# Kernel optimization log

Measured on AMD Instinct MI355X. Metric: run time of the kernel, lower is better.

## Reference

```python
import jax, jax.numpy as jnp
import numpy as np

B, N, D_IN, D_OUT, MAX_POS = 256, 256, 768, 300, 256
NEG_INF = -9e15
LEAKY_SLOPE = 0.2


def setup_inputs() -> dict:
    key = jax.random.key(0)
    ks = jax.random.split(key, 6)
    h = jax.random.normal(ks[0], (B, N, D_IN), dtype=jnp.float32)
    adj = (jax.random.uniform(ks[1], (B, N, N)) > 0.9).astype(jnp.float32)
    adj = jnp.maximum(adj, jnp.eye(N, dtype=jnp.float32)[None])
    positions = jax.random.randint(ks[2], (B, N), 0, MAX_POS)
    W = jax.random.normal(ks[3], (D_IN, D_OUT), dtype=jnp.float32) * (1.0 / np.sqrt(D_IN))
    a_src = jax.random.normal(ks[4], (1, D_OUT), dtype=jnp.float32) * 0.05
    a_dst = jax.random.normal(ks[5], (1, D_OUT), dtype=jnp.float32) * 0.05
    pos_table = jax.random.normal(jax.random.fold_in(key, 7), (MAX_POS, D_OUT), dtype=jnp.float32)
    return {"h": h, "adj": adj, "positions": positions, "W": W,
            "a_src": a_src, "a_dst": a_dst, "pos_table": pos_table}


def reference(h, adj, positions, W, a_src, a_dst, pos_table):
    # Wh = W(h) + position embedding          [B, N, D_OUT]
    Wh = jnp.einsum('bni,io->bno', h, W) + pos_table[positions]
    # additive attention scores
    f_src = jnp.einsum('bno,o->bn', Wh, a_src[0])  # [B, N]
    f_dst = jnp.einsum('bno,o->bn', Wh, a_dst[0])  # [B, N]
    e = f_src[:, :, None] + f_dst[:, None, :]      # [B, N, N]
    e = jnp.where(e >= 0, e, LEAKY_SLOPE * e)      # LeakyReLU(0.2)
    # adjacency masking + softmax over last dim
    masked = jnp.where(adj > 0, e, NEG_INF)
    attention = jax.nn.softmax(masked, axis=-1)
    # (eval mode: edge dropout and dropout are identity)
    h_prime = jnp.einsum('bnm,bmo->bno', attention, Wh)
    return h_prime, attention
```

## Files before the change

kernel.cpp:

```cpp
#include <hip/hip_runtime.h>

#define B_    256
#define N_    256
#define DIN   768
#define DOUT  300
#define DOUTP 320
#define M_    (B_*N_)
#define HP_ELEMS (M_*DOUT)
#define NEG_INF -9.0e15f

typedef _Float16 f16;
typedef __attribute__((ext_vector_type(8))) _Float16 f16x8;
typedef __attribute__((ext_vector_type(4))) _Float16 f16x4;
typedef __attribute__((ext_vector_type(4))) float    f32x4;

__device__ __forceinline__ void async_copy16(void* lds, const void* g) {
    __builtin_amdgcn_global_load_lds(
        (const __attribute__((address_space(1))) void*)g,
        (__attribute__((address_space(3))) void*)lds, 16, 0, 0);
}

__device__ __forceinline__ f16x8 cvt8(float4 u, float4 v) {
    return (f16x8){(f16)u.x,(f16)u.y,(f16)u.z,(f16)u.w,
                   (f16)v.x,(f16)v.y,(f16)v.z,(f16)v.w};
}

__global__ __launch_bounds__(256) void prep_wt(const float* __restrict__ W,
                                               f16* __restrict__ Wt) {
    int idx = blockIdx.x * 256 + threadIdx.x;
    if (idx >= DOUTP * DIN) return;
    int n = idx / DIN, k = idx - n * DIN;
    float v = (n < DOUT) ? W[k * DOUT + n] : 0.0f;
    Wt[idx] = (f16)v;
}

__global__ __launch_bounds__(256, 3) void gemm1(
    const float* __restrict__ h, const f16* __restrict__ Wt,
    const int* __restrict__ positions,
    const float* __restrict__ a_src, const float* __restrict__ a_dst,
    const float* __restrict__ pos_table,
    f16* __restrict__ WhT, float* __restrict__ f_src, float* __restrict__ f_dst)
{
    __shared__ f16 Bl[2][DOUTP * 32];
    __shared__ float pfs[64][2], pfd[64][2];

    const int tid  = threadIdx.x;
    const int wave = tid >> 6, lane = tid & 63;
    const int quad = lane >> 4, c = lane & 15;
    const int rh = wave & 1, chf = wave >> 1;
    const int rowbase = blockIdx.x * 64;

    const int brow = lane >> 2;
    const int bj   = (lane & 3) ^ (brow & 3);

    const float* hrow0 = h + (size_t)(rowbase + rh * 32 + c) * DIN + quad * 8;
    const float* hrow1 = hrow0 + 16 * DIN;

    float4 a[3][4];

#define LOAD_A(set, kt) do { \
    const float4* p0 = (const float4*)(hrow0 + (kt) * 32); \
    const float4* p1 = (const float4*)(hrow1 + (kt) * 32); \
    a[set][0] = p0[0]; a[set][1] = p0[1]; \
    a[set][2] = p1[0]; a[set][3] = p1[1]; } while (0)

#define DMA_B(buf, kt) do { \
    _Pragma("unroll") \
    for (int i_ = 0; i_ < 5; ++i_) { \
        int chk_ = wave + 4 * i_; \
        int n_ = chk_ * 16 + brow; \
        async_copy16((char*)Bl[buf] + chk_ * 1024, \
                     Wt + (size_t)n_ * DIN + (kt) * 32 + bj * 8); \
    } } while (0)

    f32x4 acc[2][10];
#pragma unroll
    for (int rt = 0; rt < 2; ++rt)
#pragma unroll
        for (int i = 0; i < 10; ++i) acc[rt][i] = (f32x4){0.f, 0.f, 0.f, 0.f};

    LOAD_A(0, 0); LOAD_A(1, 1);
    DMA_B(0, 0);  DMA_B(1, 1);
    __syncthreads();

#pragma unroll
    for (int kt = 0; kt < 24; ++kt) {
        const int cur = kt & 1;
        if (kt >= 1 && kt + 1 < 24) DMA_B(cur ^ 1, kt + 1);
        if (kt + 2 < 24) LOAD_A((kt + 2) % 3, kt + 2);

        f16x8 af0 = cvt8(a[kt % 3][0], a[kt % 3][1]);
        f16x8 af1 = cvt8(a[kt % 3][2], a[kt % 3][3]);
#pragma unroll
        for (int i = 0; i < 10; ++i) {
            int n = (chf * 10 + i) * 16 + c;
            f16x8 bf = *(const f16x8*)&Bl[cur][n * 32 + (quad ^ (n & 3)) * 8];
            acc[0][i] = __builtin_amdgcn_mfma_f32_16x16x32_f16(af0, bf, acc[0][i], 0, 0, 0);
            acc[1][i] = __builtin_amdgcn_mfma_f32_16x16x32_f16(af1, bf, acc[1][i], 0, 0, 0);
        }
        __syncthreads();
    }

    const int bidx = rowbase >> 8;
    const int mloc = rowbase & 255;

    int posr[2][4];
#pragma unroll
    for (int rt = 0; rt < 2; ++rt)
#pragma unroll
        for (int r = 0; r < 4; ++r)
            posr[rt][r] = positions[rowbase + rh * 32 + rt * 16 + quad * 4 + r];

    float fs[2][4] = {{0,0,0,0},{0,0,0,0}}, fd[2][4] = {{0,0,0,0},{0,0,0,0}};
#pragma unroll
    for (int i = 0; i < 10; ++i) {
        int col = (chf * 10 + i) * 16 + c;
        if (col < DOUT) {
            float as = a_src[col], ad = a_dst[col];
#pragma unroll
            for (int rt = 0; rt < 2; ++rt)
#pragma unroll
                for (int r = 0; r < 4; ++r) {
                    float v = acc[rt][i][r] + pos_table[posr[rt][r] * DOUT + col];
                    acc[rt][i][r] = v;
                    fs[rt][r] += v * as;
                    fd[rt][r] += v * ad;
                }
        } else {
#pragma unroll
            for (int rt = 0; rt < 2; ++rt)
#pragma unroll
                for (int r = 0; r < 4; ++r) acc[rt][i][r] = 0.0f;
        }
    }
#pragma unroll
    for (int off = 1; off < 16; off <<= 1) {
#pragma unroll
        for (int rt = 0; rt < 2; ++rt)
#pragma unroll
            for (int r = 0; r < 4; ++r) {
                fs[rt][r] += __shfl_xor(fs[rt][r], off, 16);
                fd[rt][r] += __shfl_xor(fd[rt][r], off, 16);
            }
    }
    if (c == 0) {
#pragma unroll
        for (int rt = 0; rt < 2; ++rt)
#pragma unroll
            for (int r = 0; r < 4; ++r) {
                int row = rh * 32 + rt * 16 + quad * 4 + r;
                pfs[row][chf] = fs[rt][r];
                pfd[row][chf] = fd[rt][r];
            }
    }
#pragma unroll
    for (int i = 0; i < 10; ++i) {
        int col = (chf * 10 + i) * 16 + c;
#pragma unroll
        for (int rt = 0; rt < 2; ++rt) {
            int mrow = mloc + rh * 32 + rt * 16 + quad * 4;
            f16x4 u = (f16x4){(f16)acc[rt][i][0], (f16)acc[rt][i][1],
                              (f16)acc[rt][i][2], (f16)acc[rt][i][3]};
            *(f16x4*)(WhT + ((size_t)bidx * DOUTP + col) * N_ + mrow) = u;
        }
    }
    __syncthreads();
    if (tid < 64) {
        f_src[rowbase + tid] = pfs[tid][0] + pfs[tid][1];
        f_dst[rowbase + tid] = pfd[tid][0] + pfd[tid][1];
    }
#undef LOAD_A
#undef DMA_B
}

__global__ __launch_bounds__(256, 2) void gemm2(
    const float* __restrict__ adj, const float* __restrict__ f_src,
    const float* __restrict__ f_dst, const f16* __restrict__ WhT,
    float* __restrict__ att, float* __restrict__ hp)
{
    __shared__ f16 Al[64 * 264];
    __shared__ f16 Bl[2][DOUTP * 32];

    const int tid  = threadIdx.x;
    const int wave = tid >> 6, lane = tid & 63;
    const int quad = lane >> 4, c = lane & 15;
    const int rh = wave & 1, chf = wave >> 1;
    const int rowbase = blockIdx.x * 64;
    const int bidx = rowbase >> 8;

    const int brow = lane >> 2;
    const int bj   = (lane & 3) ^ (brow & 3);

#define DMA_B2(buf, kt) do { \
    _Pragma("unroll") \
    for (int i_ = 0; i_ < 5; ++i_) { \
        int chk_ = wave + 4 * i_; \
        int n_ = chk_ * 16 + brow; \
        async_copy16((char*)Bl[buf] + chk_ * 1024, \
                     WhT + ((size_t)bidx * DOUTP + n_) * N_ + (kt) * 32 + bj * 8); \
    } } while (0)

    DMA_B2(0, 0);
    DMA_B2(1, 1);

    const int sub = lane >> 4, l16 = lane & 15;

    float4 fdv[4];
#pragma unroll
    for (int q = 0; q < 4; ++q)
        fdv[q] = *(const float4*)(f_dst + bidx * N_ + q * 64 + l16 * 4);

    float4 ar[4][4];
    int rowg[4];
#pragma unroll
    for (int g = 0; g < 4; ++g) {
        rowg[g] = rowbase + wave * 16 + g * 4 + sub;
#pragma unroll
        for (int q = 0; q < 4; ++q)
            ar[g][q] = *(const float4*)(adj + (size_t)rowg[g] * N_ + q * 64 + l16 * 4);
    }
#pragma unroll
    for (int g = 0; g < 4; ++g) {
        float fs = f_src[rowg[g]];
        float p[16];
        float mx = -3.0e38f;
#pragma unroll
        for (int q = 0; q < 4; ++q) {
            float vv[4] = {fs + fdv[q].x, fs + fdv[q].y, fs + fdv[q].z, fs + fdv[q].w};
            float aa[4] = {ar[g][q].x, ar[g][q].y, ar[g][q].z, ar[g][q].w};
#pragma unroll
            for (int j = 0; j < 4; ++j) {
                float v = vv[j];
                v = v >= 0.f ? v : 0.2f * v;
                v = aa[j] > 0.f ? v : NEG_INF;
                p[q * 4 + j] = v;
                mx = fmaxf(mx, v);
            }
        }
#pragma unroll
        for (int off = 1; off < 16; off <<= 1) mx = fmaxf(mx, __shfl_xor(mx, off, 16));
        float s = 0.f;
#pragma unroll
        for (int j = 0; j < 16; ++j) { p[j] = __expf(p[j] - mx); s += p[j]; }
#pragma unroll
        for (int off = 1; off < 16; off <<= 1) s += __shfl_xor(s, off, 16);
        float inv = 1.0f / s;
        int lr = wave * 16 + g * 4 + sub;
#pragma unroll
        for (int q = 0; q < 4; ++q) {
            float4 o = make_float4(p[q*4]*inv, p[q*4+1]*inv, p[q*4+2]*inv, p[q*4+3]*inv);
            *(float4*)(att + (size_t)rowg[g] * N_ + q * 64 + l16 * 4) = o;
            *(f16x4*)&Al[lr * 264 + q * 64 + l16 * 4] =
                (f16x4){(f16)o.x, (f16)o.y, (f16)o.z, (f16)o.w};
        }
    }

    f32x4 acc[2][10];
#pragma unroll
    for (int rt = 0; rt < 2; ++rt)
#pragma unroll
        for (int i = 0; i < 10; ++i) acc[rt][i] = (f32x4){0.f, 0.f, 0.f, 0.f};

    __syncthreads();

#pragma unroll
    for (int kt = 0; kt < 8; ++kt) {
        const int cur = kt & 1;
        if (kt >= 1 && kt + 1 < 8) DMA_B2(cur ^ 1, kt + 1);

        f16x8 af0 = *(const f16x8*)&Al[(rh * 32 + c) * 264 + kt * 32 + quad * 8];
        f16x8 af1 = *(const f16x8*)&Al[(rh * 32 + 16 + c) * 264 + kt * 32 + quad * 8];
#pragma unroll
        for (int i = 0; i < 10; ++i) {
            int n = (chf * 10 + i) * 16 + c;
            f16x8 bf = *(const f16x8*)&Bl[cur][n * 32 + (quad ^ (n & 3)) * 8];
            acc[0][i] = __builtin_amdgcn_mfma_f32_16x16x32_f16(af0, bf, acc[0][i], 0, 0, 0);
            acc[1][i] = __builtin_amdgcn_mfma_f32_16x16x32_f16(af1, bf, acc[1][i], 0, 0, 0);
        }
        __syncthreads();
    }

#pragma unroll
    for (int i = 0; i < 10; ++i) {
        int col = (chf * 10 + i) * 16 + c;
        if (col < DOUT) {
#pragma unroll
            for (int rt = 0; rt < 2; ++rt) {
                int row0 = rowbase + rh * 32 + rt * 16 + quad * 4;
#pragma unroll
                for (int r = 0; r < 4; ++r)
                    hp[(size_t)(row0 + r) * DOUT + col] = acc[rt][i][r];
            }
        }
    }
#undef DMA_B2
}

extern "C" void kernel_launch(void* const* d_in, const int* in_sizes, int n_in,
                              void* d_out, int out_size, void* d_ws, size_t ws_size,
                              hipStream_t stream)
{
    const float* h         = (const float*)d_in[0];
    const float* adj       = (const float*)d_in[1];
    const int*   positions = (const int*)d_in[2];
    const float* W         = (const float*)d_in[3];
    const float* a_src     = (const float*)d_in[4];
    const float* a_dst     = (const float*)d_in[5];
    const float* pos_table = (const float*)d_in[6];

    float* hp  = (float*)d_out;
    float* att = hp + HP_ELEMS;

    f16*   Wt    = (f16*)d_ws;
    f16*   WhT   = Wt + (size_t)DOUTP * DIN;
    float* f_src = (float*)(WhT + (size_t)B_ * DOUTP * N_);
    float* f_dst = f_src + M_;

    hipLaunchKernelGGL(prep_wt, dim3((DOUTP * DIN + 255) / 256), dim3(256), 0, stream, W, Wt);
    hipLaunchKernelGGL(gemm1,   dim3(M_ / 64), dim3(256), 0, stream,
                       h, Wt, positions, a_src, a_dst, pos_table, WhT, f_src, f_dst);
    hipLaunchKernelGGL(gemm2,   dim3(M_ / 64), dim3(256), 0, stream,
                       adj, f_src, f_dst, WhT, att, hp);
}
```

Before: 484.9 us.

## Load B operands directly from global into registers, dropping LDS staging and barriers

Both GEMM kernels stop staging the B operand (Wt and WhT tiles) in LDS through async global-to-LDS copies. Each wave now loads its own B fragments straight from global memory into double-buffered registers, and the per-iteration __syncthreads is removed. This cuts barrier and LDS traffic and frees shared memory. In exchange, every wave in a block re-reads the same B tiles from global/L2 with strided 16-byte loads, register pressure grows (gemm1 occupancy hint drops from 3 to 2), and access coalescing gets worse.

```diff
diff --git a/kernel.cpp b/kernel.cpp
--- a/kernel.cpp
+++ b/kernel.cpp
@@ -14,12 +14,6 @@
 typedef __attribute__((ext_vector_type(4))) _Float16 f16x4;
 typedef __attribute__((ext_vector_type(4))) float    f32x4;
 
-__device__ __forceinline__ void async_copy16(void* lds, const void* g) {
-    __builtin_amdgcn_global_load_lds(
-        (const __attribute__((address_space(1))) void*)g,
-        (__attribute__((address_space(3))) void*)lds, 16, 0, 0);
-}
-
 __device__ __forceinline__ f16x8 cvt8(float4 u, float4 v) {
     return (f16x8){(f16)u.x,(f16)u.y,(f16)u.z,(f16)u.w,
                    (f16)v.x,(f16)v.y,(f16)v.z,(f16)v.w};
@@ -34,14 +28,13 @@
     Wt[idx] = (f16)v;
 }
 
-__global__ __launch_bounds__(256, 3) void gemm1(
+__global__ __launch_bounds__(256, 2) void gemm1(
     const float* __restrict__ h, const f16* __restrict__ Wt,
     const int* __restrict__ positions,
     const float* __restrict__ a_src, const float* __restrict__ a_dst,
     const float* __restrict__ pos_table,
     f16* __restrict__ WhT, float* __restrict__ f_src, float* __restrict__ f_dst)
 {
-    __shared__ f16 Bl[2][DOUTP * 32];
     __shared__ float pfs[64][2], pfd[64][2];
 
     const int tid  = threadIdx.x;
@@ -50,28 +43,24 @@
     const int rh = wave & 1, chf = wave >> 1;
     const int rowbase = blockIdx.x * 64;
 
-    const int brow = lane >> 2;
-    const int bj   = (lane & 3) ^ (brow & 3);
-
     const float* hrow0 = h + (size_t)(rowbase + rh * 32 + c) * DIN + quad * 8;
     const float* hrow1 = hrow0 + 16 * DIN;
-
-    float4 a[3][4];
-
-#define LOAD_A(set, kt) do { \
-    const float4* p0 = (const float4*)(hrow0 + (kt) * 32); \
-    const float4* p1 = (const float4*)(hrow1 + (kt) * 32); \
-    a[set][0] = p0[0]; a[set][1] = p0[1]; \
-    a[set][2] = p1[0]; a[set][3] = p1[1]; } while (0)
-
-#define DMA_B(buf, kt) do { \
+    const f16* bbase = Wt + (size_t)(chf * 160 + c) * DIN + quad * 8;
+
+    float4 araw[2][4];
+    f16x8  bfr[2][10];
+
+#define LOAD_A(buf, kt) do { \
+    const float4* p0_ = (const float4*)(hrow0 + (kt) * 32); \
+    const float4* p1_ = (const float4*)(hrow1 + (kt) * 32); \
+    araw[buf][0] = p0_[0]; araw[buf][1] = p0_[1]; \
+    araw[buf][2] = p1_[0]; araw[buf][3] = p1_[1]; } while (0)
+
+#define LOAD_B(buf, kt) do { \
     _Pragma("unroll") \
-    for (int i_ = 0; i_ < 5; ++i_) { \
-        int chk_ = wave + 4 * i_; \
-        int n_ = chk_ * 16 + brow; \
-        async_copy16((char*)Bl[buf] + chk_ * 1024, \
-                     Wt + (size_t)n_ * DIN + (kt) * 32 + bj * 8); \
-    } } while (0)
+    for (int i_ = 0; i_ < 10; ++i_) \
+        bfr[buf][i_] = *(const f16x8*)(bbase + (size_t)(i_ * 16) * DIN + (kt) * 32); \
+    } while (0)
 
     f32x4 acc[2][10];
 #pragma unroll
@@ -79,27 +68,23 @@
 #pragma unroll
         for (int i = 0; i < 10; ++i) acc[rt][i] = (f32x4){0.f, 0.f, 0.f, 0.f};
 
-    LOAD_A(0, 0); LOAD_A(1, 1);
-    DMA_B(0, 0);  DMA_B(1, 1);
-    __syncthreads();
+    LOAD_A(0, 0);
+    LOAD_B(0, 0);
 
 #pragma unroll
     for (int kt = 0; kt < 24; ++kt) {
-        const int cur = kt & 1;
-        if (kt >= 1 && kt + 1 < 24) DMA_B(cur ^ 1, kt + 1);
-        if (kt + 2 < 24) LOAD_A((kt + 2) % 3, kt + 2);
-
-        f16x8 af0 = cvt8(a[kt % 3][0], a[kt % 3][1]);
-        f16x8 af1 = cvt8(a[kt % 3][2], a[kt % 3][3]);
+        const int cur = kt & 1, nxt = cur ^ 1;
+        if (kt + 1 < 24) { LOAD_B(nxt, kt + 1); LOAD_A(nxt, kt + 1); }
+        f16x8 af0 = cvt8(araw[cur][0], araw[cur][1]);
+        f16x8 af1 = cvt8(araw[cur][2], araw[cur][3]);
 #pragma unroll
         for (int i = 0; i < 10; ++i) {
-            int n = (chf * 10 + i) * 16 + c;
-            f16x8 bf = *(const f16x8*)&Bl[cur][n * 32 + (quad ^ (n & 3)) * 8];
-            acc[0][i] = __builtin_amdgcn_mfma_f32_16x16x32_f16(af0, bf, acc[0][i], 0, 0, 0);
-            acc[1][i] = __builtin_amdgcn_mfma_f32_16x16x32_f16(af1, bf, acc[1][i], 0, 0, 0);
-        }
-        __syncthreads();
-    }
+            acc[0][i] = __builtin_amdgcn_mfma_f32_16x16x32_f16(af0, bfr[cur][i], acc[0][i], 0, 0, 0);
+            acc[1][i] = __builtin_amdgcn_mfma_f32_16x16x32_f16(af1, bfr[cur][i], acc[1][i], 0, 0, 0);
+        }
+    }
+#undef LOAD_A
+#undef LOAD_B
 
     const int bidx = rowbase >> 8;
     const int mloc = rowbase & 255;
@@ -169,8 +154,6 @@
         f_src[rowbase + tid] = pfs[tid][0] + pfs[tid][1];
         f_dst[rowbase + tid] = pfd[tid][0] + pfd[tid][1];
     }
-#undef LOAD_A
-#undef DMA_B
 }
 
 __global__ __launch_bounds__(256, 2) void gemm2(
@@ -179,7 +162,6 @@
     float* __restrict__ att, float* __restrict__ hp)
 {
     __shared__ f16 Al[64 * 264];
-    __shared__ f16 Bl[2][DOUTP * 32];
 
     const int tid  = threadIdx.x;
     const int wave = tid >> 6, lane = tid & 63;
@@ -188,20 +170,16 @@
     const int rowbase = blockIdx.x * 64;
     const int bidx = rowbase >> 8;
 
-    const int brow = lane >> 2;
-    const int bj   = (lane & 3) ^ (brow & 3);
-
-#define DMA_B2(buf, kt) do { \
+    const f16* b2base = WhT + ((size_t)bidx * DOUTP + chf * 160 + c) * N_ + quad * 8;
+
+    f16x8 bfr[2][10];
+#define LOAD_B2(buf, kt) do { \
     _Pragma("unroll") \
-    for (int i_ = 0; i_ < 5; ++i_) { \
-        int chk_ = wave + 4 * i_; \
-        int n_ = chk_ * 16 + brow; \
-        async_copy16((char*)Bl[buf] + chk_ * 1024, \
-                     WhT + ((size_t)bidx * DOUTP + n_) * N_ + (kt) * 32 + bj * 8); \
-    } } while (0)
-
-    DMA_B2(0, 0);
-    DMA_B2(1, 1);
+    for (int i_ = 0; i_ < 10; ++i_) \
+        bfr[buf][i_] = *(const f16x8*)(b2base + (size_t)(i_ * 16) * N_ + (kt) * 32); \
+    } while (0)
+
+    LOAD_B2(0, 0);
 
     const int sub = lane >> 4, l16 = lane & 15;
 
@@ -265,20 +243,18 @@
 
 #pragma unroll
     for (int kt = 0; kt < 8; ++kt) {
-        const int cur = kt & 1;
-        if (kt >= 1 && kt + 1 < 8) DMA_B2(cur ^ 1, kt + 1);
+        const int cur = kt & 1, nxt = cur ^ 1;
+        if (kt + 1 < 8) LOAD_B2(nxt, kt + 1);
 
         f16x8 af0 = *(const f16x8*)&Al[(rh * 32 + c) * 264 + kt * 32 + quad * 8];
         f16x8 af1 = *(const f16x8*)&Al[(rh * 32 + 16 + c) * 264 + kt * 32 + quad * 8];
 #pragma unroll
         for (int i = 0; i < 10; ++i) {
-            int n = (chf * 10 + i) * 16 + c;
-            f16x8 bf = *(const f16x8*)&Bl[cur][n * 32 + (quad ^ (n & 3)) * 8];
-            acc[0][i] = __builtin_amdgcn_mfma_f32_16x16x32_f16(af0, bf, acc[0][i], 0, 0, 0);
-            acc[1][i] = __builtin_amdgcn_mfma_f32_16x16x32_f16(af1, bf, acc[1][i], 0, 0, 0);
-        }
-        __syncthreads();
-    }
+            acc[0][i] = __builtin_amdgcn_mfma_f32_16x16x32_f16(af0, bfr[cur][i], acc[0][i], 0, 0, 0);
+            acc[1][i] = __builtin_amdgcn_mfma_f32_16x16x32_f16(af1, bfr[cur][i], acc[1][i], 0, 0, 0);
+        }
+    }
+#undef LOAD_B2
 
 #pragma unroll
     for (int i = 0; i < 10; ++i) {
@@ -293,7 +269,6 @@
             }
         }
     }
-#undef DMA_B2
 }
 
 extern "C" void kernel_launch(void* const* d_in, const int* in_sizes, int n_in,
```

After: 560.0 us. 1.15x slower.
